# Performance work log

Measured on AMD Instinct MI355X. Metric: run time of the kernel, lower is better.

## Reference

```python
import jax, jax.numpy as jnp
import numpy as np

EMBED_DIM = 1024
NUM_HEADS = 16
HEAD_DIM = EMBED_DIM // NUM_HEADS


def setup_inputs() -> dict:
    key = jax.random.key(0)
    ks = jax.random.split(key, 9)
    B, S, E = 2, 2048, EMBED_DIM
    scale = 1.0 / np.sqrt(E)
    return {
        "query": jax.random.normal(ks[0], (B, S, E), jnp.float32),
        "key": jax.random.normal(ks[1], (B, S, E), jnp.float32),
        "value": jax.random.normal(ks[2], (B, S, E), jnp.float32),
        "wq": jax.random.normal(ks[3], (E, E), jnp.float32) * scale,
        "bq": jnp.zeros((E,), jnp.float32),
        "wk": jax.random.normal(ks[4], (E, E), jnp.float32) * scale,
        "bk": jnp.zeros((E,), jnp.float32),
        "wv": jax.random.normal(ks[5], (E, E), jnp.float32) * scale,
        "bv": jnp.zeros((E,), jnp.float32),
    }


def _split_heads(x):
    B, S, _ = x.shape
    return x.reshape(B, S, NUM_HEADS, HEAD_DIM).transpose(0, 2, 1, 3)  # [B,H,S,Dh]


def reference(query, key, value, wq, bq, wk, bk, wv, bv):
    q = _split_heads(query @ wq + bq)   # [B,H,S,Dh]
    k = _split_heads(key @ wk + bk)
    v = _split_heads(value @ wv + bv)
    logits = jnp.einsum("bhqd,bhkd->bhqk", q, k) / jnp.sqrt(
        jnp.asarray(HEAD_DIM, q.dtype)
    )
    attn = jax.nn.softmax(logits, axis=-1)          # [B,H,S,S]
    out = jnp.einsum("bhqk,bhkd->bhqd", attn, v)    # [B,H,S,Dh]
    B, H, S, Dh = out.shape
    out = out.transpose(0, 2, 1, 3).reshape(B, S, H * Dh)  # [B,S,E]
    return out, attn
```

## Files before the change

### kernel.cpp

```cpp
#include <hip/hip_runtime.h>

typedef float  f32x4  __attribute__((ext_vector_type(4)));
typedef int    i32x4  __attribute__((ext_vector_type(4)));
typedef short  bf16x8 __attribute__((ext_vector_type(8)));
typedef short  s16x4  __attribute__((ext_vector_type(4)));

#define NB   2
#define SEQ  2048
#define EMB  1024
#define NH   16
#define DH   64

__device__ inline short f2bf(float f) {
    unsigned u = __float_as_uint(f);
    u += 0x7fffu + ((u >> 16) & 1u);
    return (short)(u >> 16);
}

__device__ inline f32x4 mfma16(bf16x8 a, bf16x8 b, f32x4 c) {
    return __builtin_amdgcn_mfma_f32_16x16x32_bf16(a, b, c, 0, 0, 0);
}

__global__ __launch_bounds__(256) void wt_kernel(const float* __restrict__ w0,
                                                 const float* __restrict__ w1,
                                                 const float* __restrict__ w2,
                                                 short* __restrict__ wt) {
    __shared__ float tile[32][33];
    int blk = blockIdx.x;
    int mat = blk >> 10;
    int rem = blk & 1023;
    int kt = rem >> 5, nt = rem & 31;
    const float* W = (mat == 0) ? w0 : ((mat == 1) ? w1 : w2);
    int t = threadIdx.x;
    int row = t >> 3, c4 = (t & 7) << 2;

    f32x4 v = *(const f32x4*)(W + (kt * 32 + row) * EMB + nt * 32 + c4);
    tile[row][c4 + 0] = v[0];
    tile[row][c4 + 1] = v[1];
    tile[row][c4 + 2] = v[2];
    tile[row][c4 + 3] = v[3];
    __syncthreads();

    int n = nt * 32 + row;
    s16x4 o;
    o[0] = f2bf(tile[c4 + 0][row]);
    o[1] = f2bf(tile[c4 + 1][row]);
    o[2] = f2bf(tile[c4 + 2][row]);
    o[3] = f2bf(tile[c4 + 3][row]);
    *(s16x4*)(wt + mat * (EMB * EMB) + n * EMB + kt * 32 + c4) = o;
}

__global__ __launch_bounds__(256) void proj_kernel(const float* __restrict__ a0,
                                                   const float* __restrict__ a1,
                                                   const float* __restrict__ a2,
                                                   const float* __restrict__ b0,
                                                   const float* __restrict__ b1,
                                                   const float* __restrict__ b2,
                                                   const short* __restrict__ wt,
                                                   short* __restrict__ qkv) {
    __shared__ __align__(16) short abuf[128][72];
    __shared__ __align__(16) short wbuf[128][72];

    int orig = blockIdx.x;
    int blk = (orig & 7) * 96 + (orig >> 3);
    int mat = blk >> 8;
    int rem = blk & 255;
    int mt = rem >> 3, nt = rem & 7;

    const float* A    = (mat == 0) ? a0 : ((mat == 1) ? a1 : a2);
    const float* bias = (mat == 0) ? b0 : ((mat == 1) ? b1 : b2);
    const short* WT = wt + mat * (EMB * EMB);
    short* O = qkv + mat * (NB * SEQ * EMB);
    float scale = (mat == 0) ? 0.125f : 1.0f;

    int t = threadIdx.x;
    int lane = t & 63, w = t >> 6;
    int wr = w >> 1, wc = w & 1;
    int lg = lane >> 4, lm = lane & 15;

    int m0 = mt * 128, n0 = nt * 128;
    int srow = t >> 1, koff = (t & 1) * 32;

    f32x4 acc[4][4] = {};

    for (int k0 = 0; k0 < EMB; k0 += 64) {
        const float* ap = A + (m0 + srow) * EMB + k0 + koff;
#pragma unroll
        for (int i = 0; i < 4; i++) {
            f32x4 x = *(const f32x4*)(ap + i * 8);
            f32x4 y = *(const f32x4*)(ap + i * 8 + 4);
            bf16x8 pk;
            pk[0] = f2bf(x[0]); pk[1] = f2bf(x[1]); pk[2] = f2bf(x[2]); pk[3] = f2bf(x[3]);
            pk[4] = f2bf(y[0]); pk[5] = f2bf(y[1]); pk[6] = f2bf(y[2]); pk[7] = f2bf(y[3]);
            *(bf16x8*)&abuf[srow][koff + i * 8] = pk;
        }
        const short* wp = WT + (n0 + srow) * EMB + k0 + koff;
#pragma unroll
        for (int i = 0; i < 4; i++) {
            *(i32x4*)&wbuf[srow][koff + i * 8] = *(const i32x4*)(wp + i * 8);
        }
        __syncthreads();
#pragma unroll
        for (int ks = 0; ks < 2; ks++) {
            bf16x8 af[4], bfr[4];
#pragma unroll
            for (int mi = 0; mi < 4; mi++)
                af[mi] = *(const bf16x8*)&abuf[wr * 64 + mi * 16 + lm][ks * 32 + lg * 8];
#pragma unroll
            for (int ni = 0; ni < 4; ni++)
                bfr[ni] = *(const bf16x8*)&wbuf[wc * 64 + ni * 16 + lm][ks * 32 + lg * 8];
#pragma unroll
            for (int mi = 0; mi < 4; mi++)
#pragma unroll
                for (int ni = 0; ni < 4; ni++)
                    acc[mi][ni] = mfma16(af[mi], bfr[ni], acc[mi][ni]);
        }
        __syncthreads();
    }

    int bidx = m0 >> 11;
    if (mat == 2) {
#pragma unroll
        for (int ni = 0; ni < 4; ni++) {
            int e = n0 + wc * 64 + ni * 16 + lm;
            float bv = bias[e];
            int h = e >> 6, d = e & 63;
#pragma unroll
            for (int mi = 0; mi < 4; mi++) {
                int s = (m0 + wr * 64 + mi * 16 + lg * 4) & (SEQ - 1);
                s16x4 o;
#pragma unroll
                for (int r = 0; r < 4; r++) o[r] = f2bf(acc[mi][ni][r] + bv);
                *(s16x4*)(O + (((bidx * NH + h) * DH + d) * SEQ) + s) = o;
            }
        }
    } else {
#pragma unroll
        for (int ni = 0; ni < 4; ni++) {
            int e = n0 + wc * 64 + ni * 16 + lm;
            float bv = bias[e];
            int h = e >> 6, d = e & 63;
#pragma unroll
            for (int mi = 0; mi < 4; mi++) {
                int mrow = m0 + wr * 64 + mi * 16 + lg * 4;
#pragma unroll
                for (int r = 0; r < 4; r++) {
                    int s = (mrow + r) & (SEQ - 1);
                    float o = (acc[mi][ni][r] + bv) * scale;
                    O[((bidx * NH + h) * SEQ + s) * DH + d] = f2bf(o);
                }
            }
        }
    }
}

__global__ __launch_bounds__(256) void attn_kernel(const short* __restrict__ qkv,
                                                   float* __restrict__ out,
                                                   float* __restrict__ attn) {
    const short* Qb = qkv;
    const short* Kb = qkv + (NB * SEQ * EMB);
    const short* Vt = qkv + 2 * (NB * SEQ * EMB);

    __shared__ __align__(16) short kbuf[2][64][72];
    __shared__ __align__(16) short vbuf[2][4096];

    int orig = blockIdx.x;
    int wg = (orig & 7) * 128 + (orig >> 3);
    int bh = wg >> 5;
    int q0 = (wg & 31) * 64;
    int b = bh >> 4, hq = bh & 15;

    int t = threadIdx.x, lane = t & 63, w = t >> 6;
    int lg = lane >> 4, lm = lane & 15;
    int srow = t >> 2, sch = t & 3;

    {
        const short* qp = Qb + (bh * SEQ + q0 + srow) * DH + sch * 16;
        *(i32x4*)&kbuf[0][srow][sch * 16]     = *(const i32x4*)(qp);
        *(i32x4*)&kbuf[0][srow][sch * 16 + 8] = *(const i32x4*)(qp + 8);
    }
    __syncthreads();
    bf16x8 qf[2];
    {
        int myq = w * 16 + lm;
        qf[0] = *(const bf16x8*)&kbuf[0][myq][lg * 8];
        qf[1] = *(const bf16x8*)&kbuf[0][myq][32 + lg * 8];
    }
    __syncthreads();

    const short* kbase = Kb + (long long)bh * SEQ * DH;
    const short* vbase = Vt + (long long)bh * DH * SEQ;

    i32x4 kr0, kr1;
    {
        const short* kp = kbase + srow * DH + sch * 16;
        kr0 = *(const i32x4*)(kp); kr1 = *(const i32x4*)(kp + 8);
    }
    float rsum = 0.0f;
    for (int kt = 0; kt < 32; kt++) {
        *(i32x4*)&kbuf[kt & 1][srow][sch * 16]     = kr0;
        *(i32x4*)&kbuf[kt & 1][srow][sch * 16 + 8] = kr1;
        __syncthreads();
        if (kt < 31) {
            const short* kp = kbase + ((kt + 1) * 64 + srow) * DH + sch * 16;
            kr0 = *(const i32x4*)(kp); kr1 = *(const i32x4*)(kp + 8);
        }
#pragma unroll
        for (int ki = 0; ki < 4; ki++) {
            f32x4 s = {};
            bf16x8 kf0 = *(const bf16x8*)&kbuf[kt & 1][ki * 16 + lm][lg * 8];
            bf16x8 kf1 = *(const bf16x8*)&kbuf[kt & 1][ki * 16 + lm][32 + lg * 8];
            s = mfma16(kf0, qf[0], s);
            s = mfma16(kf1, qf[1], s);
            rsum += __expf(s[0]) + __expf(s[1]) + __expf(s[2]) + __expf(s[3]);
        }
    }
    rsum += __shfl_xor(rsum, 16);
    rsum += __shfl_xor(rsum, 32);
    float inv = 1.0f / rsum;

    f32x4 oacc[4] = {};
    float* arow = attn + ((long long)bh * SEQ + q0 + w * 16 + lm) * SEQ;

    int vA0 = (srow >> 4) * 1024 + (sch >> 1) * 512 + (srow & 15) * 8 + (sch & 1) * 4;

    i32x4 vr0, vr1;
    {
        const short* kp = kbase + srow * DH + sch * 16;
        kr0 = *(const i32x4*)(kp); kr1 = *(const i32x4*)(kp + 8);
        const short* vp = vbase + srow * SEQ + sch * 16;
        vr0 = *(const i32x4*)(vp); vr1 = *(const i32x4*)(vp + 8);
    }

    for (int kt = 0; kt < 32; kt++) {
        *(i32x4*)&kbuf[kt & 1][srow][sch * 16]     = kr0;
        *(i32x4*)&kbuf[kt & 1][srow][sch * 16 + 8] = kr1;
        union { i32x4 v; s16x4 h[2]; } u0, u1;
        u0.v = vr0; u1.v = vr1;
        *(s16x4*)&vbuf[kt & 1][vA0]       = u0.h[0];
        *(s16x4*)&vbuf[kt & 1][vA0 + 128] = u0.h[1];
        *(s16x4*)&vbuf[kt & 1][vA0 + 256] = u1.h[0];
        *(s16x4*)&vbuf[kt & 1][vA0 + 384] = u1.h[1];
        __syncthreads();
        if (kt < 31) {
            const short* kp = kbase + ((kt + 1) * 64 + srow) * DH + sch * 16;
            kr0 = *(const i32x4*)(kp); kr1 = *(const i32x4*)(kp + 8);
            const short* vp = vbase + srow * SEQ + (kt + 1) * 64 + sch * 16;
            vr0 = *(const i32x4*)(vp); vr1 = *(const i32x4*)(vp + 8);
        }

        float p[4][4];
#pragma unroll
        for (int ki = 0; ki < 4; ki++) {
            f32x4 s = {};
            bf16x8 kf0 = *(const bf16x8*)&kbuf[kt & 1][ki * 16 + lm][lg * 8];
            bf16x8 kf1 = *(const bf16x8*)&kbuf[kt & 1][ki * 16 + lm][32 + lg * 8];
            s = mfma16(kf0, qf[0], s);
            s = mfma16(kf1, qf[1], s);
#pragma unroll
            for (int r = 0; r < 4; r++) p[ki][r] = __expf(s[r]) * inv;
            f32x4 st = {p[ki][0], p[ki][1], p[ki][2], p[ki][3]};
            __builtin_nontemporal_store(st, (f32x4*)(arow + kt * 64 + ki * 16 + lg * 4));
        }

        bf16x8 pb[2];
#pragma unroll
        for (int ks = 0; ks < 2; ks++) {
            pb[ks][0] = f2bf(p[2 * ks + 0][0]);
            pb[ks][1] = f2bf(p[2 * ks + 0][1]);
            pb[ks][2] = f2bf(p[2 * ks + 0][2]);
            pb[ks][3] = f2bf(p[2 * ks + 0][3]);
            pb[ks][4] = f2bf(p[2 * ks + 1][0]);
            pb[ks][5] = f2bf(p[2 * ks + 1][1]);
            pb[ks][6] = f2bf(p[2 * ks + 1][2]);
            pb[ks][7] = f2bf(p[2 * ks + 1][3]);
        }

#pragma unroll
        for (int di = 0; di < 4; di++) {
#pragma unroll
            for (int ks = 0; ks < 2; ks++) {
                bf16x8 vf = *(const bf16x8*)&vbuf[kt & 1][(di * 2 + ks) * 512 + (lg * 16 + lm) * 8];
                oacc[di] = mfma16(vf, pb[ks], oacc[di]);
            }
        }
    }

    float* op = out + ((long long)b * SEQ + q0 + w * 16 + lm) * EMB + hq * DH;
#pragma unroll
    for (int di = 0; di < 4; di++) {
        __builtin_nontemporal_store(oacc[di], (f32x4*)(op + di * 16 + lg * 4));
    }
}

extern "C" void kernel_launch(void* const* d_in, const int* in_sizes, int n_in,
                              void* d_out, int out_size, void* d_ws, size_t ws_size,
                              hipStream_t stream) {
    const float* query = (const float*)d_in[0];
    const float* key   = (const float*)d_in[1];
    const float* value = (const float*)d_in[2];
    const float* wq    = (const float*)d_in[3];
    const float* bq    = (const float*)d_in[4];
    const float* wk    = (const float*)d_in[5];
    const float* bk    = (const float*)d_in[6];
    const float* wv    = (const float*)d_in[7];
    const float* bv    = (const float*)d_in[8];

    float* out  = (float*)d_out;
    float* attn = out + (long long)NB * SEQ * EMB;

    short* wt  = (short*)d_ws;
    short* qkv = wt + 3 * (EMB * EMB);

    hipLaunchKernelGGL(wt_kernel, dim3(3 * 1024), dim3(256), 0, stream,
                       wq, wk, wv, wt);
    hipLaunchKernelGGL(proj_kernel, dim3(3 * 256), dim3(256), 0, stream,
                       query, key, value, bq, bk, bv, wt, qkv);
    hipLaunchKernelGGL(attn_kernel, dim3(32 * 32), dim3(256), 0, stream,
                       qkv, out, attn);
}
```

Baseline: 287.1 us.

## Pre-convert activations to bf16, use exp2 softmax, packed cvt, staged QK stores

Adds a prep kernel that converts query/key/value to bf16 in workspace, when the workspace is large enough, so the projection GEMM loads bf16 tiles instead of converting fp32 in its inner loop. The Q scale now folds in log2(e) so attention can use the native exp2 instruction. Probability packing uses v_cvt_pk_bf16_f32, and the Q/K projection epilogue goes through shared memory to write coalesced 16-byte rows instead of scattered 2-byte stores. The cost is an extra full pass over the activations and more workspace.

```diff
diff --git a/kernel.cpp b/kernel.cpp
--- a/kernel.cpp
+++ b/kernel.cpp
@@ -10,6 +10,7 @@
 #define EMB  1024
 #define NH   16
 #define DH   64
+#define MATN (NB * SEQ * EMB)
 
 __device__ inline short f2bf(float f) {
     unsigned u = __float_as_uint(f);
@@ -17,40 +18,73 @@
     return (short)(u >> 16);
 }
 
+__device__ inline unsigned cvtpk(float lo, float hi) {
+    unsigned r;
+    asm("v_cvt_pk_bf16_f32 %0, %1, %2" : "=v"(r) : "v"(lo), "v"(hi));
+    return r;
+}
+
+__device__ inline float fexp2(float x) {
+#if __has_builtin(__builtin_amdgcn_exp2f)
+    return __builtin_amdgcn_exp2f(x);
+#else
+    return exp2f(x);
+#endif
+}
+
 __device__ inline f32x4 mfma16(bf16x8 a, bf16x8 b, f32x4 c) {
     return __builtin_amdgcn_mfma_f32_16x16x32_bf16(a, b, c, 0, 0, 0);
 }
 
-__global__ __launch_bounds__(256) void wt_kernel(const float* __restrict__ w0,
-                                                 const float* __restrict__ w1,
-                                                 const float* __restrict__ w2,
-                                                 short* __restrict__ wt) {
-    __shared__ float tile[32][33];
+__global__ __launch_bounds__(256) void prep_kernel(const float* __restrict__ q,
+                                                   const float* __restrict__ k,
+                                                   const float* __restrict__ v,
+                                                   const float* __restrict__ w0,
+                                                   const float* __restrict__ w1,
+                                                   const float* __restrict__ w2,
+                                                   short* __restrict__ wt,
+                                                   short* __restrict__ abf) {
     int blk = blockIdx.x;
-    int mat = blk >> 10;
-    int rem = blk & 1023;
-    int kt = rem >> 5, nt = rem & 31;
-    const float* W = (mat == 0) ? w0 : ((mat == 1) ? w1 : w2);
     int t = threadIdx.x;
-    int row = t >> 3, c4 = (t & 7) << 2;
-
-    f32x4 v = *(const f32x4*)(W + (kt * 32 + row) * EMB + nt * 32 + c4);
-    tile[row][c4 + 0] = v[0];
-    tile[row][c4 + 1] = v[1];
-    tile[row][c4 + 2] = v[2];
-    tile[row][c4 + 3] = v[3];
-    __syncthreads();
-
-    int n = nt * 32 + row;
-    s16x4 o;
-    o[0] = f2bf(tile[c4 + 0][row]);
-    o[1] = f2bf(tile[c4 + 1][row]);
-    o[2] = f2bf(tile[c4 + 2][row]);
-    o[3] = f2bf(tile[c4 + 3][row]);
-    *(s16x4*)(wt + mat * (EMB * EMB) + n * EMB + kt * 32 + c4) = o;
-}
-
-__global__ __launch_bounds__(256) void proj_kernel(const float* __restrict__ a0,
+    if (blk < 3072) {
+        __shared__ float tile[32][33];
+        int mat = blk >> 10;
+        int rem = blk & 1023;
+        int kt = rem >> 5, nt = rem & 31;
+        const float* W = (mat == 0) ? w0 : ((mat == 1) ? w1 : w2);
+        int row = t >> 3, c4 = (t & 7) << 2;
+
+        f32x4 val = *(const f32x4*)(W + (kt * 32 + row) * EMB + nt * 32 + c4);
+        tile[row][c4 + 0] = val[0];
+        tile[row][c4 + 1] = val[1];
+        tile[row][c4 + 2] = val[2];
+        tile[row][c4 + 3] = val[3];
+        __syncthreads();
+
+        int n = nt * 32 + row;
+        s16x4 o;
+        o[0] = f2bf(tile[c4 + 0][row]);
+        o[1] = f2bf(tile[c4 + 1][row]);
+        o[2] = f2bf(tile[c4 + 2][row]);
+        o[3] = f2bf(tile[c4 + 3][row]);
+        *(s16x4*)(wt + mat * (EMB * EMB) + n * EMB + kt * 32 + c4) = o;
+    } else {
+        long long i = (long long)(blk - 3072) * 2048 + t * 8;
+        int mat = (int)(i >> 22);
+        int off = (int)(i & (MATN - 1));
+        const float* A = (mat == 0) ? q : ((mat == 1) ? k : v);
+        f32x4 x = *(const f32x4*)(A + off);
+        f32x4 y = *(const f32x4*)(A + off + 4);
+        bf16x8 pk;
+        pk[0] = f2bf(x[0]); pk[1] = f2bf(x[1]); pk[2] = f2bf(x[2]); pk[3] = f2bf(x[3]);
+        pk[4] = f2bf(y[0]); pk[5] = f2bf(y[1]); pk[6] = f2bf(y[2]); pk[7] = f2bf(y[3]);
+        *(bf16x8*)(abf + i) = pk;
+    }
+}
+
+template <bool BF16A>
+__global__ __launch_bounds__(256) void proj_kernel(const short* __restrict__ abf,
+                                                   const float* __restrict__ a0,
                                                    const float* __restrict__ a1,
                                                    const float* __restrict__ a2,
                                                    const float* __restrict__ b0,
@@ -58,8 +92,9 @@
                                                    const float* __restrict__ b2,
                                                    const short* __restrict__ wt,
                                                    short* __restrict__ qkv) {
-    __shared__ __align__(16) short abuf[128][72];
-    __shared__ __align__(16) short wbuf[128][72];
+    __shared__ __align__(16) short smem[2][128][72];
+    short (*abuf)[72] = smem[0];
+    short (*wbuf)[72] = smem[1];
 
     int orig = blockIdx.x;
     int blk = (orig & 7) * 96 + (orig >> 3);
@@ -67,11 +102,12 @@
     int rem = blk & 255;
     int mt = rem >> 3, nt = rem & 7;
 
-    const float* A    = (mat == 0) ? a0 : ((mat == 1) ? a1 : a2);
     const float* bias = (mat == 0) ? b0 : ((mat == 1) ? b1 : b2);
+    const float* Af = (mat == 0) ? a0 : ((mat == 1) ? a1 : a2);
+    const short* Ab = abf + mat * MATN;
     const short* WT = wt + mat * (EMB * EMB);
-    short* O = qkv + mat * (NB * SEQ * EMB);
-    float scale = (mat == 0) ? 0.125f : 1.0f;
+    short* O = qkv + mat * MATN;
+    float scale = (mat == 0) ? 0.125f * 1.44269504f : 1.0f;
 
     int t = threadIdx.x;
     int lane = t & 63, w = t >> 6;
@@ -84,21 +120,27 @@
     f32x4 acc[4][4] = {};
 
     for (int k0 = 0; k0 < EMB; k0 += 64) {
-        const float* ap = A + (m0 + srow) * EMB + k0 + koff;
-#pragma unroll
-        for (int i = 0; i < 4; i++) {
-            f32x4 x = *(const f32x4*)(ap + i * 8);
-            f32x4 y = *(const f32x4*)(ap + i * 8 + 4);
-            bf16x8 pk;
-            pk[0] = f2bf(x[0]); pk[1] = f2bf(x[1]); pk[2] = f2bf(x[2]); pk[3] = f2bf(x[3]);
-            pk[4] = f2bf(y[0]); pk[5] = f2bf(y[1]); pk[6] = f2bf(y[2]); pk[7] = f2bf(y[3]);
-            *(bf16x8*)&abuf[srow][koff + i * 8] = pk;
+        if constexpr (BF16A) {
+            const short* ap = Ab + (m0 + srow) * EMB + k0 + koff;
+#pragma unroll
+            for (int i = 0; i < 4; i++)
+                *(i32x4*)&abuf[srow][koff + i * 8] = *(const i32x4*)(ap + i * 8);
+        } else {
+            const float* ap = Af + (m0 + srow) * EMB + k0 + koff;
+#pragma unroll
+            for (int i = 0; i < 4; i++) {
+                f32x4 x = *(const f32x4*)(ap + i * 8);
+                f32x4 y = *(const f32x4*)(ap + i * 8 + 4);
+                bf16x8 pk;
+                pk[0] = f2bf(x[0]); pk[1] = f2bf(x[1]); pk[2] = f2bf(x[2]); pk[3] = f2bf(x[3]);
+                pk[4] = f2bf(y[0]); pk[5] = f2bf(y[1]); pk[6] = f2bf(y[2]); pk[7] = f2bf(y[3]);
+                *(bf16x8*)&abuf[srow][koff + i * 8] = pk;
+            }
         }
         const short* wp = WT + (n0 + srow) * EMB + k0 + koff;
 #pragma unroll
-        for (int i = 0; i < 4; i++) {
+        for (int i = 0; i < 4; i++)
             *(i32x4*)&wbuf[srow][koff + i * 8] = *(const i32x4*)(wp + i * 8);
-        }
         __syncthreads();
 #pragma unroll
         for (int ks = 0; ks < 2; ks++) {
@@ -135,22 +177,29 @@
             }
         }
     } else {
+        short* flat = &smem[0][0][0];
 #pragma unroll
         for (int ni = 0; ni < 4; ni++) {
             int e = n0 + wc * 64 + ni * 16 + lm;
             float bv = bias[e];
-            int h = e >> 6, d = e & 63;
 #pragma unroll
             for (int mi = 0; mi < 4; mi++) {
-                int mrow = m0 + wr * 64 + mi * 16 + lg * 4;
-#pragma unroll
-                for (int r = 0; r < 4; r++) {
-                    int s = (mrow + r) & (SEQ - 1);
-                    float o = (acc[mi][ni][r] + bv) * scale;
-                    O[((bidx * NH + h) * SEQ + s) * DH + d] = f2bf(o);
-                }
+                int rr = wr * 64 + mi * 16 + lg * 4;
+#pragma unroll
+                for (int r = 0; r < 4; r++)
+                    flat[(rr + r) * 136 + wc * 64 + ni * 16 + lm] =
+                        f2bf((acc[mi][ni][r] + bv) * scale);
             }
         }
+        __syncthreads();
+        int r = t >> 1, half = t & 1;
+        int h = (n0 + half * 64) >> 6;
+        int s = (m0 + r) & (SEQ - 1);
+        short* dst = O + (((long long)bidx * NH + h) * SEQ + s) * DH;
+        const short* srcp = flat + r * 136 + half * 64;
+#pragma unroll
+        for (int j = 0; j < 8; j++)
+            *(i32x4*)(dst + j * 8) = *(const i32x4*)(srcp + j * 8);
     }
 }
 
@@ -158,8 +207,8 @@
                                                    float* __restrict__ out,
                                                    float* __restrict__ attn) {
     const short* Qb = qkv;
-    const short* Kb = qkv + (NB * SEQ * EMB);
-    const short* Vt = qkv + 2 * (NB * SEQ * EMB);
+    const short* Kb = qkv + MATN;
+    const short* Vt = qkv + 2 * MATN;
 
     __shared__ __align__(16) short kbuf[2][64][72];
     __shared__ __align__(16) short vbuf[2][4096];
@@ -212,7 +261,7 @@
             bf16x8 kf1 = *(const bf16x8*)&kbuf[kt & 1][ki * 16 + lm][32 + lg * 8];
             s = mfma16(kf0, qf[0], s);
             s = mfma16(kf1, qf[1], s);
-            rsum += __expf(s[0]) + __expf(s[1]) + __expf(s[2]) + __expf(s[3]);
+            rsum += fexp2(s[0]) + fexp2(s[1]) + fexp2(s[2]) + fexp2(s[3]);
         }
     }
     rsum += __shfl_xor(rsum, 16);
@@ -258,7 +307,7 @@
             s = mfma16(kf0, qf[0], s);
             s = mfma16(kf1, qf[1], s);
 #pragma unroll
-            for (int r = 0; r < 4; r++) p[ki][r] = __expf(s[r]) * inv;
+            for (int r = 0; r < 4; r++) p[ki][r] = fexp2(s[r]) * inv;
             f32x4 st = {p[ki][0], p[ki][1], p[ki][2], p[ki][3]};
             __builtin_nontemporal_store(st, (f32x4*)(arow + kt * 64 + ki * 16 + lg * 4));
         }
@@ -266,14 +315,12 @@
         bf16x8 pb[2];
 #pragma unroll
         for (int ks = 0; ks < 2; ks++) {
-            pb[ks][0] = f2bf(p[2 * ks + 0][0]);
-            pb[ks][1] = f2bf(p[2 * ks + 0][1]);
-            pb[ks][2] = f2bf(p[2 * ks + 0][2]);
-            pb[ks][3] = f2bf(p[2 * ks + 0][3]);
-            pb[ks][4] = f2bf(p[2 * ks + 1][0]);
-            pb[ks][5] = f2bf(p[2 * ks + 1][1]);
-            pb[ks][6] = f2bf(p[2 * ks + 1][2]);
-            pb[ks][7] = f2bf(p[2 * ks + 1][3]);
+            union { unsigned d[4]; bf16x8 v; } u;
+            u.d[0] = cvtpk(p[2 * ks + 0][0], p[2 * ks + 0][1]);
+            u.d[1] = cvtpk(p[2 * ks + 0][2], p[2 * ks + 0][3]);
+            u.d[2] = cvtpk(p[2 * ks + 1][0], p[2 * ks + 1][1]);
+            u.d[3] = cvtpk(p[2 * ks + 1][2], p[2 * ks + 1][3]);
+            pb[ks] = u.v;
         }
 
 #pragma unroll
@@ -309,13 +356,22 @@
     float* out  = (float*)d_out;
     float* attn = out + (long long)NB * SEQ * EMB;
 
+    size_t need_full = ((size_t)3 * EMB * EMB + 6ull * MATN) * sizeof(short);
+    bool bf16a = ws_size >= need_full;
+
     short* wt  = (short*)d_ws;
-    short* qkv = wt + 3 * (EMB * EMB);
-
-    hipLaunchKernelGGL(wt_kernel, dim3(3 * 1024), dim3(256), 0, stream,
-                       wq, wk, wv, wt);
-    hipLaunchKernelGGL(proj_kernel, dim3(3 * 256), dim3(256), 0, stream,
-                       query, key, value, bq, bk, bv, wt, qkv);
-    hipLaunchKernelGGL(attn_kernel, dim3(32 * 32), dim3(256), 0, stream,
+    short* abf = wt + 3 * (EMB * EMB);
+    short* qkv = bf16a ? (abf + 3 * MATN) : abf;
+
+    hipLaunchKernelGGL(prep_kernel, dim3(bf16a ? 9216 : 3072), dim3(256), 0, stream,
+                       query, key, value, wq, wk, wv, wt, abf);
+    if (bf16a) {
+        hipLaunchKernelGGL((proj_kernel<true>), dim3(768), dim3(256), 0, stream,
+                           abf, query, key, value, bq, bk, bv, wt, qkv);
+    } else {
+        hipLaunchKernelGGL((proj_kernel<false>), dim3(768), dim3(256), 0, stream,
+                           abf, query, key, value, bq, bk, bv, wt, qkv);
+    }
+    hipLaunchKernelGGL(attn_kernel, dim3(1024), dim3(256), 0, stream,
                        qkv, out, attn);
 }
```

Measured after the change: 268.8 us. -6.4%, faster.
